# Kernel optimization log

Hardware: AMD Instinct MI355X
Metric: run time of the kernel (lower is better)

The kernel has to match this reference:

```python
import jax, jax.numpy as jnp
import numpy as np

BS, L, ED = 4, 2048, 1024
D = ED // 2          # time_embedding_dim = 512
ANG_HID = D // 4     # AngleEmb hidden = 128
T_MAX = 1010


def _gelu(x):
    return jax.nn.gelu(x, approximate=False)  # torch F.gelu default = exact erf


def _time_embed(t, w1, b1, w2, b2):
    # sinusoidal (diffusion-style, base 10000) + 2-layer MLP; t: [N] float
    half = D // 2
    freqs = jnp.exp(-jnp.log(10000.0) * jnp.arange(half, dtype=jnp.float32) / half)
    a = t[:, None] * freqs[None, :]
    e = jnp.concatenate([jnp.sin(a), jnp.cos(a)], axis=-1)  # [N, D]
    return _gelu(e @ w1 + b1) @ w2 + b2


def _cal_dist(p, aa_seq):
    # p: [bs, L, 3]; ragged per-segment mean pairwise distance.
    # Segments run (cls_idx+1 .. eos_idx-1]; token 0 = cls, token 2 = eos.
    cls = (aa_seq == 0)
    eos = (aa_seq == 2)
    seg = jnp.cumsum(cls.astype(jnp.int32), axis=1)                       # segment id
    valid = (seg > jnp.cumsum(eos.astype(jnp.int32), axis=1)) & ~cls & ~eos
    same = (seg[:, :, None] == seg[:, None, :]) & valid[:, :, None] & valid[:, None, :]
    diff = p[:, :, None, :] - p[:, None, :, :]                            # [bs,L,L,3]
    sq = jnp.sum(diff * diff, axis=-1)
    d = jnp.where(sq > 0, jnp.sqrt(jnp.where(sq > 0, sq, 1.0)), 0.0)      # safe norm
    cnt = jnp.sum(same, axis=-1)                                           # segment size (incl self)
    dist = jnp.where(valid, jnp.sum(d * same, axis=-1) / jnp.maximum(cnt, 1), 0.0)
    return dist[..., None]                                                 # [bs,L,1]


def setup_inputs() -> dict:
    key = jax.random.key(0)
    ks = jax.random.split(key, 26)
    # build ragged aa_seq: repeated [cls=0, residues in [3,25), eos=2], pad token 1
    rng = np.random.default_rng(0)
    aa = np.ones((BS, L), dtype=np.int64)
    pad = np.ones((BS, L), dtype=bool)
    for b in range(BS):
        i = 0
        while i < L - 8:
            seg = int(rng.integers(16, 64))
            seg = min(seg, L - i - 2)
            aa[b, i] = 0
            aa[b, i + 1:i + 1 + seg] = rng.integers(3, 25, size=seg)
            aa[b, i + 1 + seg] = 2
            pad[b, i:i + 2 + seg] = False
            i += seg + 2
    s = 0.05
    inp = {
        "pos": jax.random.normal(ks[0], (BS, L, 3, 3), jnp.float32) * 5.0,
        "angle": jax.random.uniform(ks[1], (BS, L, 6), jnp.float32, -3.14, 3.14),
        "padding_mask": jnp.asarray(pad),
        "mask_aa": jax.random.bernoulli(ks[2], 0.15, (BS, L, 1)),
        "mask_pos": jax.random.bernoulli(ks[3], 0.15, (BS, L, 1)),
        "mask_angle": jax.random.bernoulli(ks[4], 0.15, (BS, L, 1)),
        "angle_mask": jax.random.bernoulli(ks[5], 0.9, (BS, L, 3)),
        "bond_angle_mask": jax.random.bernoulli(ks[6], 0.9, (BS, L, 3)),
        "time_pos": jax.random.randint(ks[7], (BS, L), 0, T_MAX).astype(jnp.float32),
        "time_angle": jnp.zeros((BS, L, 6), jnp.float32),  # overwritten in fwd (dim-2 path)
        "aa_seq": jnp.asarray(aa),
        # parameters ([in, out] layout; torch Linear bias=False unless noted)
        "ang_w1": jax.random.normal(ks[8], (1, ANG_HID), jnp.float32) * 0.5,
        "ang_w2": jax.random.normal(ks[9], (ANG_HID, D), jnp.float32) * s,
        "pos_w1": jax.random.normal(ks[10], (1, 1), jnp.float32) * 0.5,
        "pos_w2": jax.random.normal(ks[11], (1, D), jnp.float32) * s,
        "te_w1": jax.random.normal(ks[12], (D, D), jnp.float32) * s,
        "te_b1": jnp.zeros((D,), jnp.float32),
        "te_w2": jax.random.normal(ks[13], (D, D), jnp.float32) * s,
        "te_b2": jnp.zeros((D,), jnp.float32),
        "angproj_w": jax.random.normal(ks[14], (6 * D, D), jnp.float32) * s,
        "angproj_b": jnp.zeros((D,), jnp.float32),
        "posproj_w": jax.random.normal(ks[15], (D, D), jnp.float32) * s,
        "posproj_b": jnp.zeros((D,), jnp.float32),
        "cls_w": jax.random.normal(ks[16], (1, ED), jnp.float32) * s,
        "eos_w": jax.random.normal(ks[17], (1, ED), jnp.float32) * s,
        "unkang_w": jax.random.normal(ks[18], (1, D), jnp.float32) * s,
        "unkpos_w": jax.random.normal(ks[19], (1, D), jnp.float32) * s,
    }
    return inp


def reference(pos, angle, padding_mask, mask_aa, mask_pos, mask_angle,
              angle_mask, bond_angle_mask, time_pos, time_angle, aa_seq,
              ang_w1, ang_w2, pos_w1, pos_w2,
              te_w1, te_b1, te_w2, te_b2,
              angproj_w, angproj_b, posproj_w, posproj_b,
              cls_w, eos_w, unkang_w, unkpos_w):
    bs, nnode, _ = angle.shape
    amask = jnp.concatenate([angle_mask[:, :, :3], bond_angle_mask], axis=-1)  # [bs,L,6]
    ang = jnp.where(amask, angle, 0.0).reshape(bs, -1, 1)                      # [bs,6L,1]
    cls_mask = (aa_seq == 0)[..., None]
    eos_mask = (aa_seq == 2)[..., None]

    angle_feat = _gelu(ang @ ang_w1) @ ang_w2                                  # [bs,6L,D]
    angle_feat = jnp.where(amask.reshape(bs, -1, 1), angle_feat, unkang_w[0])

    dist = _cal_dist(pos[:, :, 1, :], aa_seq)                                  # [bs,L,1]
    pos_feat = _gelu(dist @ pos_w1) @ pos_w2                                   # [bs,L,D]
    pos_mask = ~(cls_mask | eos_mask)
    pos_feat = jnp.where(pos_mask, pos_feat, unkpos_w[0])

    # time_pos is 2-D -> [bs,L,1]; time_angle := time_pos repeated to [bs,L,6]
    ta = jnp.where(amask, jnp.broadcast_to(time_pos[..., None], (bs, nnode, 6)), 0.0)
    temb_pos = _time_embed(time_pos.reshape(-1), te_w1, te_b1, te_w2, te_b2).reshape(bs, -1, D)
    temb_ang = _time_embed(ta.reshape(-1), te_w1, te_b1, te_w2, te_b2).reshape(bs, -1, D)
    t0_emb = _time_embed(jnp.zeros((1,), jnp.float32), te_w1, te_b1, te_w2, te_b2)[0]  # all-zero t rows are identical

    t_mask = mask_angle & ~cls_mask & ~eos_mask                                # [bs,L,1]
    temb_ang = jnp.where(jnp.tile(t_mask, (1, 6, 1)), temb_ang, t0_emb)        # torch .repeat(1,6,1)
    temb_pos = jnp.where(t_mask, temb_pos, t0_emb)
    angle_feat = angle_feat + temb_ang
    pos_feat = pos_feat + temb_pos

    angle_feat = angle_feat.reshape(bs, nnode, 6 * D) @ angproj_w + angproj_b  # [bs,L,D]
    pos_feat = pos_feat @ posproj_w + posproj_b                                # [bs,L,D]
    node = jnp.concatenate([angle_feat, pos_feat], axis=-1)                    # [bs,L,ED]
    node = jnp.where(cls_mask, cls_w[0], node)
    node = jnp.where(eos_mask, eos_w[0], node)
    node = jnp.where(padding_mask[..., None], 0.0, node)
    return node
```

## Files before the change

kernel.cpp:

```cpp
#include <hip/hip_runtime.h>
#include <hip/hip_bf16.h>
#include <cstdint>
#include <cstddef>

#define BSZ 4
#define SEQL 2048
#define DDIM 512
#define AHID 128
#define NROWS (BSZ*SEQL)
#define NANG (NROWS*6)
#define KCAT 768
#define NTT 1024
#define YCAP 4096

typedef __attribute__((ext_vector_type(8))) short short8;
typedef __attribute__((ext_vector_type(4))) float f32x4;
typedef __hip_bfloat16 bf16;

__device__ __forceinline__ float gelu_f(float x){
  return 0.5f * x * (1.0f + erff(x * 0.7071067811865475f));
}

__device__ __forceinline__ void gload16(const void* g, void* l){
  __builtin_amdgcn_global_load_lds(
      (const __attribute__((address_space(1))) unsigned int*)g,
      (__attribute__((address_space(3))) unsigned int*)l,
      16, 0, 0);
}

__device__ __forceinline__ unsigned int packbf2(float a, float b){
  __hip_bfloat16 ha = __float2bfloat16(a), hb = __float2bfloat16(b);
  return (unsigned int)(*(unsigned short*)&ha) | ((unsigned int)(*(unsigned short*)&hb) << 16);
}

__global__ void pre_kernel(const int* __restrict__ aa, const float* __restrict__ pos,
                           float4* __restrict__ pk,
                           const float* __restrict__ te_w1, const float* __restrict__ te_b1,
                           const float* __restrict__ te_w2, const float* __restrict__ te_b2,
                           const float* __restrict__ angproj_w, const float* __restrict__ posproj_w,
                           const float* __restrict__ unkang, const float* __restrict__ pos_w2,
                           float* __restrict__ t0, float* __restrict__ U,
                           float* __restrict__ Wg, float* __restrict__ qb){
  int blk = blockIdx.x, tid = threadIdx.x;
  if (blk == 0){
    int b = tid >> 6, lane = tid & 63;
    const int CH = SEQL/64;
    int base = b*SEQL + lane*CH;
    int av[CH];
    int lc=0, le=0;
    #pragma unroll
    for (int i=0;i<CH;i++){ int a=aa[base+i]; av[i]=a; lc += (a==0); le += (a==2); }
    int pc=lc, pe=le;
    #pragma unroll
    for (int off=1; off<64; off<<=1){
      int tc = __shfl_up(pc, off);
      int te = __shfl_up(pe, off);
      if (lane >= off){ pc += tc; pe += te; }
    }
    int c = pc - lc, eo = pe - le;
    #pragma unroll
    for (int i=0;i<CH;i++){
      int a = av[i];
      c += (a==0); eo += (a==2);
      bool valid = (c>eo) && (a!=0) && (a!=2);
      float4 q;
      q.x = pos[(size_t)(base+i)*9+3];
      q.y = pos[(size_t)(base+i)*9+4];
      q.z = pos[(size_t)(base+i)*9+5];
      q.w = valid ? (float)c : -1.f;
      pk[base+i] = q;
    }
    return;
  }
  int q = blk - 1;
  if (q < 32){
    __shared__ float zsh[8][32];
    __shared__ float hsh[32];
    int nc = q >> 4, dc = q & 15;
    int d0 = dc * 32;
    int dl = tid & 31, kc = tid >> 5;
    float p = 0.f;
    #pragma unroll 4
    for (int i=0;i<32;i++)
      p += te_w1[(size_t)(256 + kc*32 + i)*512 + d0 + dl];
    zsh[kc][dl] = p;
    __syncthreads();
    if (tid < 32){
      float z = te_b1[d0 + tid];
      #pragma unroll
      for (int k=0;k<8;k++) z += zsh[k][tid];
      hsh[tid] = gelu_f(z);
    }
    __syncthreads();
    int n = nc*256 + tid;
    float s = (dc==0) ? te_b2[n] : 0.f;
    #pragma unroll 4
    for (int i=0;i<32;i++)
      s += hsh[i] * te_w2[(size_t)(d0+i)*512 + n];
    atomicAdd(t0 + n, s);
    return;
  }
  q -= 32;
  if (q < 96){
    int j = q >> 4, rem = q & 15;
    int nc = rem >> 3, dc = rem & 7;
    int n = nc*256 + tid, d0 = dc*64;
    float s = 0.f;
    #pragma unroll 4
    for (int i=0;i<64;i++)
      s += unkang[d0+i] * angproj_w[((size_t)(j*512 + d0+i))*512 + n];
    atomicAdd(U + j*512 + n, s);
    return;
  }
  q -= 96;
  if (q < 16){
    int nc = q >> 3, dc = q & 7;
    int n = nc*256 + tid, d0 = dc*64;
    float s = 0.f;
    #pragma unroll 4
    for (int i=0;i<64;i++)
      s += pos_w2[d0+i] * posproj_w[(size_t)(d0+i)*512 + n];
    atomicAdd(Wg + n, s);
    return;
  }
  q -= 16;
  {
    int j = q >> 4, rem = q & 15;
    int nc = rem >> 3, dc = rem & 7;
    int n = nc*256 + tid, d0 = dc*64;
    const float* W = (j<6) ? (angproj_w + (size_t)(j*512)*512) : posproj_w;
    float s = 0.f;
    #pragma unroll 4
    for (int i=0;i<64;i++)
      s += te_b2[d0+i] * W[(size_t)(d0+i)*512 + n];
    atomicAdd(qb + j*512 + n, s);
  }
}

#define NB_ANGH 3072
#define NB_SIN  256
#define NB_TR   2208
#define NB_PREP 32
#define NB_CONST 112
#define NB_DIST 2048
#define NB_TOTAL (NB_ANGH+NB_SIN+NB_TR+NB_PREP+NB_CONST+NB_DIST)

__device__ void do_transpose(const float* __restrict__ W, bf16* __restrict__ Wt,
                             int K, int q, float (*tsh)[33]){
  int k0 = (q >> 4)*32, n0 = (q & 15)*32;
  int tx = threadIdx.x & 31, ty = threadIdx.x >> 5;
  #pragma unroll
  for (int i=0;i<32;i+=8)
    tsh[ty+i][tx] = W[(size_t)(k0+ty+i)*512 + n0+tx];
  __syncthreads();
  #pragma unroll
  for (int i=0;i<32;i+=8)
    Wt[(size_t)(n0+ty+i)*K + k0+tx] = __float2bfloat16(tsh[tx][ty+i]);
}

__device__ __forceinline__ void wave_append(int j, bool q, int bl,
                                            int* __restrict__ cnts, int* __restrict__ lists,
                                            int* __restrict__ posi){
  unsigned long long m = __ballot(q);
  if (m){
    int lane = threadIdx.x & 63;
    int lead = __ffsll((long long)m) - 1;
    int base = 0;
    if (lane == lead) base = atomicAdd(&cnts[j], __popcll(m));
    base = __shfl(base, lead);
    if (q){
      int pre = __popcll(m & ((1ull<<lane)-1ull));
      int p = base + pre;
      lists[j*NROWS + p] = bl;
      posi[j*NROWS + bl] = p;
    }
  }
}

__global__ void prologue_kernel(const float* __restrict__ angle,
                                const int* __restrict__ angm, const int* __restrict__ bondm,
                                const int* __restrict__ mask_angle, const int* __restrict__ aa,
                                const int* __restrict__ padm,
                                const float* __restrict__ ang_w1,
                                const float* __restrict__ te_w1, const float* __restrict__ te_w2,
                                const float* __restrict__ ang_w2, const float* __restrict__ angproj_w,
                                const float* __restrict__ posproj_w,
                                const float4* __restrict__ pk, const float* __restrict__ t0,
                                bf16* __restrict__ Hang, bf16* __restrict__ et,
                                bf16* __restrict__ tw1t, bf16* __restrict__ apjt,
                                bf16* __restrict__ ppjt, bf16* __restrict__ w2b,
                                bf16* __restrict__ tw2b,
                                unsigned char* __restrict__ amb, unsigned char* __restrict__ scb,
                                int* __restrict__ cnts, int* __restrict__ lists,
                                int* __restrict__ posi,
                                float* __restrict__ dist,
                                float* __restrict__ V, float* __restrict__ Wt0){
  __shared__ float tsh[32][33];
  int blk = blockIdx.x;
  int tid = threadIdx.x;
  if (blk < NB_ANGH){
    int gidx = blk*256 + tid;
    int row = gidx >> 4;
    int kb = (gidx & 15) * 8;
    int bq = row / (SEQL*6);
    int rr = row - bq*(SEQL*6);
    int l = rr / 6, j = rr - l*6;
    int bl = bq*SEQL + l;
    int m = (j<3) ? angm[bl*3+j] : bondm[bl*3+(j-3)];
    float x = m ? angle[bl*6+j] : 0.f;
    float4 w0 = *(const float4*)(ang_w1+kb);
    float4 w1v = *(const float4*)(ang_w1+kb+4);
    uint4 st;
    st.x = packbf2(gelu_f(x*w0.x),  gelu_f(x*w0.y));
    st.y = packbf2(gelu_f(x*w0.z),  gelu_f(x*w0.w));
    st.z = packbf2(gelu_f(x*w1v.x), gelu_f(x*w1v.y));
    st.w = packbf2(gelu_f(x*w1v.z), gelu_f(x*w1v.w));
    *(uint4*)(Hang + (size_t)row*AHID + kb) = st;
    return;
  }
  blk -= NB_ANGH;
  if (blk < NB_SIN){
    int gidx = blk*256 + tid;
    int row = gidx >> 6;
    int db = (gidx & 63) * 8;
    float t = (float)row;
    float v[8];
    #pragma unroll
    for (int i=0;i<8;i++){
      int d = db + i;
      int k = d & 255;
      float f = exp2f(-0.05190512648262f * (float)k);
      float a = t * f;
      v[i] = (d < 256) ? __sinf(a) : __cosf(a);
    }
    uint4 st;
    st.x = packbf2(v[0],v[1]); st.y = packbf2(v[2],v[3]);
    st.z = packbf2(v[4],v[5]); st.w = packbf2(v[6],v[7]);
    *(uint4*)(et + (size_t)row*DDIM + db) = st;
    return;
  }
  blk -= NB_SIN;
  if (blk < NB_TR){
    if (blk < 256)       do_transpose(te_w1, tw1t, 512, blk, tsh);
    else if (blk < 1792) do_transpose(angproj_w, apjt, 3072, blk-256, tsh);
    else if (blk < 2048) do_transpose(posproj_w, ppjt, 512, blk-1792, tsh);
    else if (blk < 2080){
      int gidx = (blk-2048)*256 + tid;
      float4 a0 = *(const float4*)(ang_w2 + (size_t)gidx*8);
      float4 a1 = *(const float4*)(ang_w2 + (size_t)gidx*8 + 4);
      uint4 st;
      st.x = packbf2(a0.x,a0.y); st.y = packbf2(a0.z,a0.w);
      st.z = packbf2(a1.x,a1.y); st.w = packbf2(a1.z,a1.w);
      *(uint4*)(w2b + (size_t)gidx*8) = st;
    } else {
      int gidx = (blk-2080)*256 + tid;
      float4 a0 = *(const float4*)(te_w2 + (size_t)gidx*8);
      float4 a1 = *(const float4*)(te_w2 + (size_t)gidx*8 + 4);
      uint4 st;
      st.x = packbf2(a0.x,a0.y); st.y = packbf2(a0.z,a0.w);
      st.z = packbf2(a1.x,a1.y); st.w = packbf2(a1.z,a1.w);
      *(uint4*)(tw2b + (size_t)gidx*8) = st;
    }
    return;
  }
  blk -= NB_TR;
  if (blk < NB_PREP){
    int bl = blk*256 + tid;
    int b = bl >> 11, l = bl & (SEQL-1);
    int a = aa[bl];
    bool rowOK = (a!=0) && (a!=2) && (padm[bl]==0);
    int ab=0, sb=0;
    #pragma unroll
    for (int j=0;j<6;j++){
      int am = (j<3) ? angm[bl*3+j] : bondm[bl*3+(j-3)];
      int rr = l*6 + j;
      int bl2 = b*SEQL + (rr & (SEQL-1));
      int a2 = aa[bl2];
      bool tm = mask_angle[bl2] && (a2!=0) && (a2!=2);
      bool qs = tm && (am!=0) && rowOK;
      if (am)  ab |= (1<<j);
      if (qs)  sb |= (1<<j);
      wave_append(j, qs, bl, cnts, lists, posi);
    }
    bool q6 = (mask_angle[bl]!=0) && rowOK;
    if (q6) sb |= 64;
    wave_append(6, q6, bl, cnts, lists, posi);
    amb[bl] = (unsigned char)ab;
    scb[bl] = (unsigned char)sb;
    return;
  }
  blk -= NB_PREP;
  if (blk < NB_CONST){
    int j = blk >> 4, rem = blk & 15;
    int nc = rem >> 3, dc = rem & 7;
    int n = nc*256 + tid, d0 = dc*64;
    const float* W = (j<6) ? (angproj_w + (size_t)(j*512)*512) : posproj_w;
    float* dst = (j<6) ? (V + j*512) : Wt0;
    float s = 0.f;
    #pragma unroll 4
    for (int i=0;i<64;i++)
      s += t0[d0+i] * W[(size_t)(d0+i)*512 + n];
    atomicAdd(dst + n, s);
    return;
  }
  blk -= NB_CONST;
  {
    int gw = blk*4 + (tid >> 6);
    int lane = tid & 63;
    float4 c = pk[gw];
    float out = 0.f;
    if (c.w >= 0.f){
      int rowbase = (gw >> 11) << 11;
      int jlo = gw - 64; if (jlo < rowbase) jlo = rowbase;
      int jhi = gw + 64; if (jhi >= rowbase + SEQL) jhi = rowbase + SEQL - 1;
      float s = 0.f, cnt = 0.f;
      for (int j = gw - 64 + lane; j <= jhi; j += 64){
        if (j < jlo) continue;
        float4 q = pk[j];
        if (q.w == c.w){
          float dx = c.x-q.x, dy = c.y-q.y, dz = c.z-q.z;
          float sq = dx*dx+dy*dy+dz*dz;
          s += (sq>0.f) ? sqrtf(sq) : 0.f;
          cnt += 1.f;
        }
      }
      #pragma unroll
      for (int off=32; off>0; off>>=1){
        s   += __shfl_down(s, off);
        cnt += __shfl_down(cnt, off);
      }
      out = s / fmaxf(cnt, 1.f);
    }
    if (lane==0) dist[gw] = out;
  }
}

struct EpiArgs {
  const float* bias;
  const unsigned char* amb;
  const unsigned char* scb;
  const float* U;
  const float* V;
  const float* Y;
  const int* posi;
  const int* aa;
  const int* pad;
  const float* cls;
  const float* eos;
  float* outF;
  bf16* outB;
  int cnt;
  int coloff;
  int ldc;
};

#define STG_BYTES 12288
#define SMEM_BYTES 49152

template<int EPI>
__device__ __forceinline__ void gemm_core(const char* gA, const char* gB,
                                          int K, int bm, int bn, const EpiArgs& ea, char* smem){
  const int tid = threadIdx.x;
  const int w = tid >> 6, lane = tid & 63;
  const bool doB = (w < 4);
  const int wm = (w>>1)*32, wn = (w&1)*32;
  const int lm = lane & 15, kq = lane >> 4;
  const int sw = kq ^ ((lm>>1)&3);
  const int NT = K >> 5;

  f32x4 acc[2][2];
  #pragma unroll
  for (int i=0;i<2;i++)
    #pragma unroll
    for (int j=0;j<2;j++) acc[i][j] = (f32x4){0.f,0.f,0.f,0.f};

  #pragma unroll
  for (int s=0; s<3; ++s){
    char* base = smem + s*STG_BYTES;
    gload16(gA + (size_t)s*64, base + w*1024);
    if (doB) gload16(gB + (size_t)s*64, base + 8192 + w*1024);
  }

  for (int t = 0; t < NT; ++t){
    char* cur = smem + (t&3)*STG_BYTES;
    if (t+3 < NT){
      char* nxt = smem + ((t+3)&3)*STG_BYTES;
      gload16(gA + (size_t)(t+3)*64, nxt + w*1024);
      if (doB) gload16(gB + (size_t)(t+3)*64, nxt + 8192 + w*1024);
    }
    int ia = NT-1-t; if (ia > 3) ia = 3;
    if (doB){
      if      (ia==3) __asm__ volatile("s_waitcnt vmcnt(6)" ::: "memory");
      else if (ia==2) __asm__ volatile("s_waitcnt vmcnt(4)" ::: "memory");
      else if (ia==1) __asm__ volatile("s_waitcnt vmcnt(2)" ::: "memory");
      else            __asm__ volatile("s_waitcnt vmcnt(0)" ::: "memory");
    } else {
      if      (ia==3) __asm__ volatile("s_waitcnt vmcnt(3)" ::: "memory");
      else if (ia==2) __asm__ volatile("s_waitcnt vmcnt(2)" ::: "memory");
      else if (ia==1) __asm__ volatile("s_waitcnt vmcnt(1)" ::: "memory");
      else            __asm__ volatile("s_waitcnt vmcnt(0)" ::: "memory");
    }
    __builtin_amdgcn_s_barrier();
    short8 af[2], bfr[2];
    #pragma unroll
    for (int tt=0;tt<2;tt++) af[tt]  = *(const short8*)(cur + (wm+tt*16+lm)*64 + sw*16);
    #pragma unroll
    for (int tt=0;tt<2;tt++) bfr[tt] = *(const short8*)(cur + 8192 + (wn+tt*16+lm)*64 + sw*16);
    #pragma unroll
    for (int mt=0;mt<2;mt++)
      #pragma unroll
      for (int nt=0;nt<2;nt++)
        acc[mt][nt] = __builtin_amdgcn_mfma_f32_16x16x32_bf16(af[mt], bfr[nt], acc[mt][nt], 0, 0, 0);
    __builtin_amdgcn_s_barrier();
  }

  float* eps = (float*)smem + w*576;
  const int erow = lane >> 2;
  const int ecg  = (lane & 3) * 8;
  #pragma unroll
  for (int mt=0; mt<2; mt++){
    #pragma unroll
    for (int nt=0; nt<2; nt++)
      #pragma unroll
      for (int rr=0; rr<4; rr++)
        eps[(kq*4+rr)*36 + nt*16 + lm] = acc[mt][nt][rr];
    __asm__ volatile("s_waitcnt lgkmcnt(0)" ::: "memory");
    float4 t0v = *(float4*)(eps + erow*36 + ecg);
    float4 t1v = *(float4*)(eps + erow*36 + ecg + 4);
    float v[8] = {t0v.x,t0v.y,t0v.z,t0v.w,t1v.x,t1v.y,t1v.z,t1v.w};
    __asm__ volatile("s_waitcnt lgkmcnt(0)" ::: "memory");
    int row = bm + wm + mt*16 + erow;
    int col = bn + wn + ecg;

    if (EPI==0 || EPI==1){
      float4 b0 = *(const float4*)(ea.bias+col), b1 = *(const float4*)(ea.bias+col+4);
      float bb[8] = {b0.x,b0.y,b0.z,b0.w,b1.x,b1.y,b1.z,b1.w};
      #pragma unroll
      for (int i=0;i<8;i++){
        v[i] += bb[i];
        if (EPI==0) v[i] = gelu_f(v[i]);
      }
      uint4 st;
      st.x = packbf2(v[0],v[1]); st.y = packbf2(v[2],v[3]);
      st.z = packbf2(v[4],v[5]); st.w = packbf2(v[6],v[7]);
      *(uint4*)(ea.outB + (size_t)row*ea.ldc + col) = st;
    } else if (EPI==4){
      uint4 st;
      st.x = packbf2(v[0],v[1]); st.y = packbf2(v[2],v[3]);
      st.z = packbf2(v[4],v[5]); st.w = packbf2(v[6],v[7]);
      *(uint4*)(ea.outB + (size_t)row*ea.ldc + col + ea.coloff) = st;
    } else if (EPI==5){
      float4 b0 = *(const float4*)(ea.bias+col), b1 = *(const float4*)(ea.bias+col+4);
      v[0]+=b0.x; v[1]+=b0.y; v[2]+=b0.z; v[3]+=b0.w;
      v[4]+=b1.x; v[5]+=b1.y; v[6]+=b1.z; v[7]+=b1.w;
      int ab = ea.amb[row], sc = ea.scb[row];
      #pragma unroll
      for (int j=0;j<6;j++){
        float mU = ((ab>>j)&1) ? 0.f : 1.f;
        float mV = ((sc>>j)&1) ? 0.f : 1.f;
        const float* Up = ea.U + j*512 + col;
        const float* Vp = ea.V + j*512 + col;
        float4 u0=*(const float4*)Up, u1=*(const float4*)(Up+4);
        float4 w0=*(const float4*)Vp, w1=*(const float4*)(Vp+4);
        v[0]+=mU*u0.x+mV*w0.x; v[1]+=mU*u0.y+mV*w0.y;
        v[2]+=mU*u0.z+mV*w0.z; v[3]+=mU*u0.w+mV*w0.w;
        v[4]+=mU*u1.x+mV*w1.x; v[5]+=mU*u1.y+mV*w1.y;
        v[6]+=mU*u1.z+mV*w1.z; v[7]+=mU*u1.w+mV*w1.w;
      }
      if (sc & 63){
        #pragma unroll
        for (int j=0;j<6;j++){
          if ((sc>>j)&1){
            const float* yp = ea.Y + ((size_t)j*YCAP + ea.posi[j*NROWS+row])*512 + col;
            float4 y0 = *(const float4*)yp, y1 = *(const float4*)(yp+4);
            v[0]+=y0.x; v[1]+=y0.y; v[2]+=y0.z; v[3]+=y0.w;
            v[4]+=y1.x; v[5]+=y1.y; v[6]+=y1.z; v[7]+=y1.w;
          }
        }
      }
      int a = ea.aa[row];
      if (a==0){
        float4 c0 = *(const float4*)(ea.cls+col), c1 = *(const float4*)(ea.cls+col+4);
        v[0]=c0.x;v[1]=c0.y;v[2]=c0.z;v[3]=c0.w;v[4]=c1.x;v[5]=c1.y;v[6]=c1.z;v[7]=c1.w;
      } else if (a==2){
        float4 c0 = *(const float4*)(ea.eos+col), c1 = *(const float4*)(ea.eos+col+4);
        v[0]=c0.x;v[1]=c0.y;v[2]=c0.z;v[3]=c0.w;v[4]=c1.x;v[5]=c1.y;v[6]=c1.z;v[7]=c1.w;
      }
      if (ea.pad[row]){
        #pragma unroll
        for (int i=0;i<8;i++) v[i]=0.f;
      }
      *(float4*)(ea.outF + (size_t)row*ea.ldc + col)     = make_float4(v[0],v[1],v[2],v[3]);
      *(float4*)(ea.outF + (size_t)row*ea.ldc + col + 4) = make_float4(v[4],v[5],v[6],v[7]);
    } else {
      if (row < ea.cnt){
        float4 b0 = *(const float4*)(ea.bias+col), b1 = *(const float4*)(ea.bias+col+4);
        v[0]+=b0.x; v[1]+=b0.y; v[2]+=b0.z; v[3]+=b0.w;
        v[4]+=b1.x; v[5]+=b1.y; v[6]+=b1.z; v[7]+=b1.w;
        float* dst = ea.outF + (size_t)row*ea.ldc + col;
        *(float4*)dst     = make_float4(v[0],v[1],v[2],v[3]);
        *(float4*)(dst+4) = make_float4(v[4],v[5],v[6],v[7]);
      }
    }
  }
}

__device__ __forceinline__ void mk_addrs(const bf16* A, size_t lda, int bm,
                                         const bf16* Bt, size_t ldb, int bn,
                                         const char*& gA, const char*& gB){
  int tid = threadIdx.x;
  int w = tid >> 6, lane = tid & 63;
  int r = w*16 + (lane>>2);
  int cg = (lane&3) ^ ((r>>1)&3);
  gA = (const char*)(A + (size_t)(bm+r)*lda + cg*8);
  gB = (const char*)(Bt + (size_t)(bn+r)*ldb + cg*8);
}

__launch_bounds__(512, 8)
__global__ void te1_wcat_q_kernel(const bf16* __restrict__ et, const bf16* __restrict__ tw1t,
                                  EpiArgs eaH,
                                  const bf16* __restrict__ apjt, const bf16* __restrict__ ppjt,
                                  const bf16* __restrict__ w2b, const bf16* __restrict__ tw2b,
                                  EpiArgs eaW, bf16* __restrict__ QT){
  __shared__ __align__(16) char smem[SMEM_BYTES];
  int id = blockIdx.x;
  const char *gA, *gB;
  if (id < 64){
    int m = id >> 3, n = id & 7;
    mk_addrs(et, 512, m*128, tw1t, 512, n*64, gA, gB);
    gemm_core<0>(gA, gB, 512, m*128, n*64, eaH, smem);
  } else if (id < 112){
    int q = id - 64;
    int j = q >> 3, m = (q >> 1) & 3, n = q & 1;
    mk_addrs(apjt, 3072, m*128, w2b, 512, n*64, gA, gB);
    gA += (size_t)j*512*2;
    eaW.coloff = j*128;
    gemm_core<4>(gA, gB, 512, m*128, n*64, eaW, smem);
  } else {
    int q = id - 112;
    int j = q >> 5, rem = q & 31;
    int m = rem >> 3, n = rem & 7;
    if (j < 6){
      mk_addrs(apjt, 3072, m*128, tw2b, 512, n*64, gA, gB);
      gA += (size_t)j*512*2;
    } else {
      mk_addrs(ppjt, 512, m*128, tw2b, 512, n*64, gA, gB);
    }
    EpiArgs ea{};
    ea.outB = QT + (size_t)j*DDIM*DDIM; ea.ldc = DDIM; ea.coloff = 0;
    gemm_core<4>(gA, gB, 512, m*128, n*64, ea, smem);
  }
}

__launch_bounds__(512, 8)
__global__ void sparse_kernel(const bf16* __restrict__ H1, const bf16* __restrict__ QT,
                              const float* __restrict__ qb, const float* __restrict__ time_pos,
                              const int* __restrict__ cnts, const int* __restrict__ lists,
                              float* __restrict__ Y){
  __shared__ __align__(16) char smem[SMEM_BYTES];
  int id = blockIdx.x;
  int jj = id >> 8, q = id & 255;
  int mt = q >> 3, nt = q & 7;
  int cnt = cnts[jj];
  if (cnt > YCAP) cnt = YCAP;
  if (mt*128 >= cnt) return;
  const int* idx = lists + jj*NROWS;
  int tid = threadIdx.x;
  int w = tid >> 6, lane = tid & 63;
  int r = w*16 + (lane>>2);
  int cg = (lane&3) ^ ((r>>1)&3);
  int ar = mt*128 + r; if (ar >= cnt) ar = cnt-1;
  int ti = (int)time_pos[idx[ar]];
  const char* gA = (const char*)(H1 + (size_t)ti*DDIM + cg*8);
  const char* gB = (const char*)(QT + (size_t)jj*DDIM*DDIM + (size_t)(nt*64+r)*DDIM + cg*8);
  EpiArgs ea{};
  ea.bias = qb + jj*512;
  ea.cnt = cnt;
  ea.outF = Y + (size_t)jj*YCAP*512;
  ea.ldc = 512;
  gemm_core<7>(gA, gB, 512, mt*128, nt*64, ea, smem);
}

__launch_bounds__(512, 8)
__global__ void proj_kernel(const bf16* __restrict__ Hang, const bf16* __restrict__ Wcat,
                            EpiArgs eaA,
                            const int* __restrict__ aa, const int* __restrict__ padm,
                            const unsigned char* __restrict__ scb, const int* __restrict__ posi,
                            const float* __restrict__ Y,
                            const float* __restrict__ dist,
                            const float* __restrict__ pw1, const float* __restrict__ Wg,
                            const float* __restrict__ Wt0, const float* __restrict__ bp,
                            const float* __restrict__ cls, const float* __restrict__ eos,
                            float* __restrict__ out){
  __shared__ __align__(16) char smem[SMEM_BYTES];
  int id = blockIdx.x;
  if (id < 512){
    int c = id & 7, q = id >> 3;
    int n = q & 7, mh = q >> 3;
    int m = mh*8 + c;
    const char *gA, *gB;
    mk_addrs(Hang, KCAT, m*128, Wcat, KCAT, n*64, gA, gB);
    gemm_core<5>(gA, gB, KCAT, m*128, n*64, eaA, smem);
    return;
  }
  int gidx = (id-512)*512 + threadIdx.x;
  int row = gidx >> 6;
  int db = (gidx & 63) * 8;
  int a = aa[row];
  float v[8];
  if (a==0 || a==2){
    const float* src = ((a==0) ? cls : eos) + DDIM + db;
    float4 c0 = *(const float4*)src, c1 = *(const float4*)(src+4);
    v[0]=c0.x;v[1]=c0.y;v[2]=c0.z;v[3]=c0.w;v[4]=c1.x;v[5]=c1.y;v[6]=c1.z;v[7]=c1.w;
  } else {
    int sc = scb[row];
    float g = gelu_f(dist[row]*pw1[0]);
    float tmul = (sc & 64) ? 0.f : 1.f;
    float4 g0 = *(const float4*)(Wg+db),  g1 = *(const float4*)(Wg+db+4);
    float4 w0 = *(const float4*)(Wt0+db), w1 = *(const float4*)(Wt0+db+4);
    float4 b0 = *(const float4*)(bp+db),  b1 = *(const float4*)(bp+db+4);
    v[0]=g*g0.x+tmul*w0.x+b0.x; v[1]=g*g0.y+tmul*w0.y+b0.y;
    v[2]=g*g0.z+tmul*w0.z+b0.z; v[3]=g*g0.w+tmul*w0.w+b0.w;
    v[4]=g*g1.x+tmul*w1.x+b1.x; v[5]=g*g1.y+tmul*w1.y+b1.y;
    v[6]=g*g1.z+tmul*w1.z+b1.z; v[7]=g*g1.w+tmul*w1.w+b1.w;
    if (sc & 64){
      const float* yp = Y + ((size_t)6*YCAP + posi[6*NROWS+row])*512 + db;
      float4 y0 = *(const float4*)yp, y1 = *(const float4*)(yp+4);
      v[0]+=y0.x; v[1]+=y0.y; v[2]+=y0.z; v[3]+=y0.w;
      v[4]+=y1.x; v[5]+=y1.y; v[6]+=y1.z; v[7]+=y1.w;
    }
  }
  if (padm[row]){
    #pragma unroll
    for (int i=0;i<8;i++) v[i]=0.f;
  }
  float* dst = out + (size_t)row*1024 + DDIM + db;
  *(float4*)dst     = make_float4(v[0],v[1],v[2],v[3]);
  *(float4*)(dst+4) = make_float4(v[4],v[5],v[6],v[7]);
}

extern "C" void kernel_launch(void* const* d_in, const int* in_sizes, int n_in,
                              void* d_out, int out_size, void* d_ws, size_t ws_size,
                              hipStream_t stream){
  const float* pos        = (const float*)d_in[0];
  const float* angle      = (const float*)d_in[1];
  const int*   padm       = (const int*)d_in[2];
  const int*   mask_angle = (const int*)d_in[5];
  const int*   angle_mask = (const int*)d_in[6];
  const int*   bond_mask  = (const int*)d_in[7];
  const float* time_pos   = (const float*)d_in[8];
  const int*   aa         = (const int*)d_in[10];
  const float* ang_w1     = (const float*)d_in[11];
  const float* ang_w2     = (const float*)d_in[12];
  const float* pos_w1     = (const float*)d_in[13];
  const float* pos_w2     = (const float*)d_in[14];
  const float* te_w1      = (const float*)d_in[15];
  const float* te_b1      = (const float*)d_in[16];
  const float* te_w2      = (const float*)d_in[17];
  const float* te_b2      = (const float*)d_in[18];
  const float* angproj_w  = (const float*)d_in[19];
  const float* angproj_b  = (const float*)d_in[20];
  const float* posproj_w  = (const float*)d_in[21];
  const float* posproj_b  = (const float*)d_in[22];
  const float* cls_w      = (const float*)d_in[23];
  const float* eos_w      = (const float*)d_in[24];
  const float* unkang     = (const float*)d_in[25];

  char* ws = (char*)d_ws;
  size_t off = 0;
  auto alloc = [&](size_t bytes)->char*{
    char* p = ws + off;
    off += (bytes + 255) & ~(size_t)255;
    return p;
  };
  int*   cnts   = (int*)  alloc(256);
  float* t0     = (float*)alloc((size_t)DDIM*4);
  float* U      = (float*)alloc((size_t)6*DDIM*4);
  float* V      = (float*)alloc((size_t)6*DDIM*4);
  float* Wt0    = (float*)alloc((size_t)DDIM*4);
  float* Wg     = (float*)alloc((size_t)DDIM*4);
  float* qb     = (float*)alloc((size_t)7*DDIM*4);
  size_t zbytes = (size_t)((char*)qb - (char*)cnts) + 7*DDIM*4;
  float* dist   = (float*)alloc((size_t)NROWS*4);
  float4* pk    = (float4*)alloc((size_t)NROWS*16);
  unsigned char* amb  = (unsigned char*)alloc(NROWS);
  unsigned char* scb  = (unsigned char*)alloc(NROWS);
  int*   lists  = (int*)  alloc((size_t)7*NROWS*4);
  int*   posi   = (int*)  alloc((size_t)7*NROWS*4);
  bf16*  et     = (bf16*) alloc((size_t)NTT*DDIM*2);
  bf16*  H1     = (bf16*) alloc((size_t)NTT*DDIM*2);
  bf16*  Hang   = (bf16*) alloc((size_t)NANG*AHID*2);
  bf16*  tw1t   = (bf16*) alloc((size_t)DDIM*DDIM*2);
  bf16*  apjt   = (bf16*) alloc((size_t)DDIM*6*DDIM*2);
  bf16*  ppjt   = (bf16*) alloc((size_t)DDIM*DDIM*2);
  bf16*  w2b    = (bf16*) alloc((size_t)AHID*DDIM*2);
  bf16*  tw2b   = (bf16*) alloc((size_t)DDIM*DDIM*2);
  bf16*  Wcat   = (bf16*) alloc((size_t)DDIM*KCAT*2);
  bf16*  QT     = (bf16*) alloc((size_t)7*DDIM*DDIM*2);
  float* Y      = (float*)alloc((size_t)7*YCAP*512*4);

  float* out = (float*)d_out;
  dim3 b256(256), b512(512);

  hipMemsetAsync(cnts, 0, zbytes, stream);

  pre_kernel<<<dim3(257), b256, 0, stream>>>(aa, pos, pk,
      te_w1, te_b1, te_w2, te_b2, angproj_w, posproj_w, unkang, pos_w2,
      t0, U, Wg, qb);

  prologue_kernel<<<dim3(NB_TOTAL), b256, 0, stream>>>(
      angle, angle_mask, bond_mask, mask_angle, aa, padm, ang_w1,
      te_w1, te_w2, ang_w2, angproj_w, posproj_w, pk, t0,
      Hang, et, tw1t, apjt, ppjt, w2b, tw2b, amb, scb, cnts, lists, posi,
      dist, V, Wt0);

  EpiArgs eaH{}; eaH.bias = te_b1; eaH.outB = H1; eaH.ldc = DDIM;
  EpiArgs eaW{}; eaW.outB = Wcat; eaW.ldc = KCAT;
  te1_wcat_q_kernel<<<dim3(336), b512, 0, stream>>>(et, tw1t, eaH,
      apjt, ppjt, w2b, tw2b, eaW, QT);

  sparse_kernel<<<dim3(7*256), b512, 0, stream>>>(H1, QT, qb, time_pos,
      cnts, lists, Y);

  EpiArgs eaA{};
  eaA.bias = angproj_b; eaA.amb = amb; eaA.scb = scb; eaA.U = U; eaA.V = V;
  eaA.Y = Y; eaA.posi = posi;
  eaA.aa = aa; eaA.pad = padm; eaA.cls = cls_w; eaA.eos = eos_w;
  eaA.outF = out; eaA.ldc = 1024;
  proj_kernel<<<dim3(1536), b512, 0, stream>>>(Hang, Wcat, eaA,
      aa, padm, scb, posi, Y, dist, pos_w1, Wg, Wt0, posproj_b, cls_w, eos_w, out);
}
```

Baseline: 210.2 us.

## Precompute projected time-embedding table over all timesteps and gather by index

```diff
diff --git a/kernel.cpp b/kernel.cpp
--- a/kernel.cpp
+++ b/kernel.cpp
@@ -11,7 +11,6 @@
 #define NANG (NROWS*6)
 #define KCAT 768
 #define NTT 1024
-#define YCAP 4096
 
 typedef __attribute__((ext_vector_type(8))) short short8;
 typedef __attribute__((ext_vector_type(4))) float f32x4;
@@ -35,12 +34,11 @@
 
 __global__ void pre_kernel(const int* __restrict__ aa, const float* __restrict__ pos,
                            float4* __restrict__ pk,
-                           const float* __restrict__ te_w1, const float* __restrict__ te_b1,
-                           const float* __restrict__ te_w2, const float* __restrict__ te_b2,
+                           const float* __restrict__ te_b2,
                            const float* __restrict__ angproj_w, const float* __restrict__ posproj_w,
                            const float* __restrict__ unkang, const float* __restrict__ pos_w2,
-                           float* __restrict__ t0, float* __restrict__ U,
-                           float* __restrict__ Wg, float* __restrict__ qb){
+                           float* __restrict__ U, float* __restrict__ Wg,
+                           float* __restrict__ qb){
   int blk = blockIdx.x, tid = threadIdx.x;
   if (blk == 0){
     int b = tid >> 6, lane = tid & 63;
@@ -73,34 +71,6 @@
     return;
   }
   int q = blk - 1;
-  if (q < 32){
-    __shared__ float zsh[8][32];
-    __shared__ float hsh[32];
-    int nc = q >> 4, dc = q & 15;
-    int d0 = dc * 32;
-    int dl = tid & 31, kc = tid >> 5;
-    float p = 0.f;
-    #pragma unroll 4
-    for (int i=0;i<32;i++)
-      p += te_w1[(size_t)(256 + kc*32 + i)*512 + d0 + dl];
-    zsh[kc][dl] = p;
-    __syncthreads();
-    if (tid < 32){
-      float z = te_b1[d0 + tid];
-      #pragma unroll
-      for (int k=0;k<8;k++) z += zsh[k][tid];
-      hsh[tid] = gelu_f(z);
-    }
-    __syncthreads();
-    int n = nc*256 + tid;
-    float s = (dc==0) ? te_b2[n] : 0.f;
-    #pragma unroll 4
-    for (int i=0;i<32;i++)
-      s += hsh[i] * te_w2[(size_t)(d0+i)*512 + n];
-    atomicAdd(t0 + n, s);
-    return;
-  }
-  q -= 32;
   if (q < 96){
     int j = q >> 4, rem = q & 15;
     int nc = rem >> 3, dc = rem & 7;
@@ -141,9 +111,8 @@
 #define NB_SIN  256
 #define NB_TR   2208
 #define NB_PREP 32
-#define NB_CONST 112
 #define NB_DIST 2048
-#define NB_TOTAL (NB_ANGH+NB_SIN+NB_TR+NB_PREP+NB_CONST+NB_DIST)
+#define NB_TOTAL (NB_ANGH+NB_SIN+NB_TR+NB_PREP+NB_DIST)
 
 __device__ void do_transpose(const float* __restrict__ W, bf16* __restrict__ Wt,
                              int K, int q, float (*tsh)[33]){
@@ -158,25 +127,6 @@
     Wt[(size_t)(n0+ty+i)*K + k0+tx] = __float2bfloat16(tsh[tx][ty+i]);
 }
 
-__device__ __forceinline__ void wave_append(int j, bool q, int bl,
-                                            int* __restrict__ cnts, int* __restrict__ lists,
-                                            int* __restrict__ posi){
-  unsigned long long m = __ballot(q);
-  if (m){
-    int lane = threadIdx.x & 63;
-    int lead = __ffsll((long long)m) - 1;
-    int base = 0;
-    if (lane == lead) base = atomicAdd(&cnts[j], __popcll(m));
-    base = __shfl(base, lead);
-    if (q){
-      int pre = __popcll(m & ((1ull<<lane)-1ull));
-      int p = base + pre;
-      lists[j*NROWS + p] = bl;
-      posi[j*NROWS + bl] = p;
-    }
-  }
-}
-
 __global__ void prologue_kernel(const float* __restrict__ angle,
                                 const int* __restrict__ angm, const int* __restrict__ bondm,
                                 const int* __restrict__ mask_angle, const int* __restrict__ aa,
@@ -185,16 +135,13 @@
                                 const float* __restrict__ te_w1, const float* __restrict__ te_w2,
                                 const float* __restrict__ ang_w2, const float* __restrict__ angproj_w,
                                 const float* __restrict__ posproj_w,
-                                const float4* __restrict__ pk, const float* __restrict__ t0,
+                                const float4* __restrict__ pk,
                                 bf16* __restrict__ Hang, bf16* __restrict__ et,
                                 bf16* __restrict__ tw1t, bf16* __restrict__ apjt,
                                 bf16* __restrict__ ppjt, bf16* __restrict__ w2b,
                                 bf16* __restrict__ tw2b,
                                 unsigned char* __restrict__ amb, unsigned char* __restrict__ scb,
-                                int* __restrict__ cnts, int* __restrict__ lists,
-                                int* __restrict__ posi,
-                                float* __restrict__ dist,
-                                float* __restrict__ V, float* __restrict__ Wt0){
+                                float* __restrict__ dist){
   __shared__ float tsh[32][33];
   int blk = blockIdx.x;
   int tid = threadIdx.x;
@@ -280,30 +227,13 @@
       bool qs = tm && (am!=0) && rowOK;
       if (am)  ab |= (1<<j);
       if (qs)  sb |= (1<<j);
-      wave_append(j, qs, bl, cnts, lists, posi);
-    }
-    bool q6 = (mask_angle[bl]!=0) && rowOK;
-    if (q6) sb |= 64;
-    wave_append(6, q6, bl, cnts, lists, posi);
+    }
+    if ((mask_angle[bl]!=0) && rowOK) sb |= 64;
     amb[bl] = (unsigned char)ab;
     scb[bl] = (unsigned char)sb;
     return;
   }
   blk -= NB_PREP;
-  if (blk < NB_CONST){
-    int j = blk >> 4, rem = blk & 15;
-    int nc = rem >> 3, dc = rem & 7;
-    int n = nc*256 + tid, d0 = dc*64;
-    const float* W = (j<6) ? (angproj_w + (size_t)(j*512)*512) : posproj_w;
-    float* dst = (j<6) ? (V + j*512) : Wt0;
-    float s = 0.f;
-    #pragma unroll 4
-    for (int i=0;i<64;i++)
-      s += t0[d0+i] * W[(size_t)(d0+i)*512 + n];
-    atomicAdd(dst + n, s);
-    return;
-  }
-  blk -= NB_CONST;
   {
     int gw = blk*4 + (tid >> 6);
     int lane = tid & 63;
@@ -340,9 +270,8 @@
   const unsigned char* amb;
   const unsigned char* scb;
   const float* U;
-  const float* V;
   const float* Y;
-  const int* posi;
+  const float* tp;
   const int* aa;
   const int* pad;
   const float* cls;
@@ -454,29 +383,19 @@
       v[0]+=b0.x; v[1]+=b0.y; v[2]+=b0.z; v[3]+=b0.w;
       v[4]+=b1.x; v[5]+=b1.y; v[6]+=b1.z; v[7]+=b1.w;
       int ab = ea.amb[row], sc = ea.scb[row];
+      int trow = (int)ea.tp[row];
       #pragma unroll
       for (int j=0;j<6;j++){
         float mU = ((ab>>j)&1) ? 0.f : 1.f;
-        float mV = ((sc>>j)&1) ? 0.f : 1.f;
         const float* Up = ea.U + j*512 + col;
-        const float* Vp = ea.V + j*512 + col;
         float4 u0=*(const float4*)Up, u1=*(const float4*)(Up+4);
-        float4 w0=*(const float4*)Vp, w1=*(const float4*)(Vp+4);
-        v[0]+=mU*u0.x+mV*w0.x; v[1]+=mU*u0.y+mV*w0.y;
-        v[2]+=mU*u0.z+mV*w0.z; v[3]+=mU*u0.w+mV*w0.w;
-        v[4]+=mU*u1.x+mV*w1.x; v[5]+=mU*u1.y+mV*w1.y;
-        v[6]+=mU*u1.z+mV*w1.z; v[7]+=mU*u1.w+mV*w1.w;
-      }
-      if (sc & 63){
-        #pragma unroll
-        for (int j=0;j<6;j++){
-          if ((sc>>j)&1){
-            const float* yp = ea.Y + ((size_t)j*YCAP + ea.posi[j*NROWS+row])*512 + col;
-            float4 y0 = *(const float4*)yp, y1 = *(const float4*)(yp+4);
-            v[0]+=y0.x; v[1]+=y0.y; v[2]+=y0.z; v[3]+=y0.w;
-            v[4]+=y1.x; v[5]+=y1.y; v[6]+=y1.z; v[7]+=y1.w;
-          }
-        }
+        int idx = ((sc>>j)&1) ? trow : 0;
+        const float* yp = ea.Y + ((size_t)j*NTT + idx)*512 + col;
+        float4 y0=*(const float4*)yp, y1=*(const float4*)(yp+4);
+        v[0]+=mU*u0.x+y0.x; v[1]+=mU*u0.y+y0.y;
+        v[2]+=mU*u0.z+y0.z; v[3]+=mU*u0.w+y0.w;
+        v[4]+=mU*u1.x+y1.x; v[5]+=mU*u1.y+y1.y;
+        v[6]+=mU*u1.z+y1.z; v[7]+=mU*u1.w+y1.w;
       }
       int a = ea.aa[row];
       if (a==0){
@@ -553,30 +472,18 @@
 }
 
 __launch_bounds__(512, 8)
-__global__ void sparse_kernel(const bf16* __restrict__ H1, const bf16* __restrict__ QT,
-                              const float* __restrict__ qb, const float* __restrict__ time_pos,
-                              const int* __restrict__ cnts, const int* __restrict__ lists,
-                              float* __restrict__ Y){
+__global__ void yt_kernel(const bf16* __restrict__ H1, const bf16* __restrict__ QT,
+                          const float* __restrict__ qb, float* __restrict__ YT){
   __shared__ __align__(16) char smem[SMEM_BYTES];
   int id = blockIdx.x;
-  int jj = id >> 8, q = id & 255;
-  int mt = q >> 3, nt = q & 7;
-  int cnt = cnts[jj];
-  if (cnt > YCAP) cnt = YCAP;
-  if (mt*128 >= cnt) return;
-  const int* idx = lists + jj*NROWS;
-  int tid = threadIdx.x;
-  int w = tid >> 6, lane = tid & 63;
-  int r = w*16 + (lane>>2);
-  int cg = (lane&3) ^ ((r>>1)&3);
-  int ar = mt*128 + r; if (ar >= cnt) ar = cnt-1;
-  int ti = (int)time_pos[idx[ar]];
-  const char* gA = (const char*)(H1 + (size_t)ti*DDIM + cg*8);
-  const char* gB = (const char*)(QT + (size_t)jj*DDIM*DDIM + (size_t)(nt*64+r)*DDIM + cg*8);
+  int jj = id >> 6, rem = id & 63;
+  int mt = rem >> 3, nt = rem & 7;
+  const char *gA, *gB;
+  mk_addrs(H1, 512, mt*128, QT + (size_t)jj*DDIM*DDIM, 512, nt*64, gA, gB);
   EpiArgs ea{};
   ea.bias = qb + jj*512;
-  ea.cnt = cnt;
-  ea.outF = Y + (size_t)jj*YCAP*512;
+  ea.cnt = NTT;
+  ea.outF = YT + (size_t)jj*NTT*512;
   ea.ldc = 512;
   gemm_core<7>(gA, gB, 512, mt*128, nt*64, ea, smem);
 }
@@ -585,11 +492,11 @@
 __global__ void proj_kernel(const bf16* __restrict__ Hang, const bf16* __restrict__ Wcat,
                             EpiArgs eaA,
                             const int* __restrict__ aa, const int* __restrict__ padm,
-                            const unsigned char* __restrict__ scb, const int* __restrict__ posi,
-                            const float* __restrict__ Y,
-                            const float* __restrict__ dist,
+                            const unsigned char* __restrict__ scb,
+                            const float* __restrict__ YT,
+                            const float* __restrict__ dist, const float* __restrict__ time_pos,
                             const float* __restrict__ pw1, const float* __restrict__ Wg,
-                            const float* __restrict__ Wt0, const float* __restrict__ bp,
+                            const float* __restrict__ bp,
                             const float* __restrict__ cls, const float* __restrict__ eos,
                             float* __restrict__ out){
   __shared__ __align__(16) char smem[SMEM_BYTES];
@@ -615,20 +522,15 @@
   } else {
     int sc = scb[row];
     float g = gelu_f(dist[row]*pw1[0]);
-    float tmul = (sc & 64) ? 0.f : 1.f;
+    int idx = (sc & 64) ? (int)time_pos[row] : 0;
+    const float* yp = YT + ((size_t)6*NTT + idx)*512 + db;
     float4 g0 = *(const float4*)(Wg+db),  g1 = *(const float4*)(Wg+db+4);
-    float4 w0 = *(const float4*)(Wt0+db), w1 = *(const float4*)(Wt0+db+4);
+    float4 y0 = *(const float4*)yp,       y1 = *(const float4*)(yp+4);
     float4 b0 = *(const float4*)(bp+db),  b1 = *(const float4*)(bp+db+4);
-    v[0]=g*g0.x+tmul*w0.x+b0.x; v[1]=g*g0.y+tmul*w0.y+b0.y;
-    v[2]=g*g0.z+tmul*w0.z+b0.z; v[3]=g*g0.w+tmul*w0.w+b0.w;
-    v[4]=g*g1.x+tmul*w1.x+b1.x; v[5]=g*g1.y+tmul*w1.y+b1.y;
-    v[6]=g*g1.z+tmul*w1.z+b1.z; v[7]=g*g1.w+tmul*w1.w+b1.w;
-    if (sc & 64){
-      const float* yp = Y + ((size_t)6*YCAP + posi[6*NROWS+row])*512 + db;
-      float4 y0 = *(const float4*)yp, y1 = *(const float4*)(yp+4);
-      v[0]+=y0.x; v[1]+=y0.y; v[2]+=y0.z; v[3]+=y0.w;
-      v[4]+=y1.x; v[5]+=y1.y; v[6]+=y1.z; v[7]+=y1.w;
-    }
+    v[0]=g*g0.x+y0.x+b0.x; v[1]=g*g0.y+y0.y+b0.y;
+    v[2]=g*g0.z+y0.z+b0.z; v[3]=g*g0.w+y0.w+b0.w;
+    v[4]=g*g1.x+y1.x+b1.x; v[5]=g*g1.y+y1.y+b1.y;
+    v[6]=g*g1.z+y1.z+b1.z; v[7]=g*g1.w+y1.w+b1.w;
   }
   if (padm[row]){
     #pragma unroll
@@ -673,20 +575,14 @@
     off += (bytes + 255) & ~(size_t)255;
     return p;
   };
-  int*   cnts   = (int*)  alloc(256);
-  float* t0     = (float*)alloc((size_t)DDIM*4);
   float* U      = (float*)alloc((size_t)6*DDIM*4);
-  float* V      = (float*)alloc((size_t)6*DDIM*4);
-  float* Wt0    = (float*)alloc((size_t)DDIM*4);
   float* Wg     = (float*)alloc((size_t)DDIM*4);
   float* qb     = (float*)alloc((size_t)7*DDIM*4);
-  size_t zbytes = (size_t)((char*)qb - (char*)cnts) + 7*DDIM*4;
+  size_t zbytes = (size_t)((char*)qb - (char*)U) + 7*DDIM*4;
   float* dist   = (float*)alloc((size_t)NROWS*4);
   float4* pk    = (float4*)alloc((size_t)NROWS*16);
   unsigned char* amb  = (unsigned char*)alloc(NROWS);
   unsigned char* scb  = (unsigned char*)alloc(NROWS);
-  int*   lists  = (int*)  alloc((size_t)7*NROWS*4);
-  int*   posi   = (int*)  alloc((size_t)7*NROWS*4);
   bf16*  et     = (bf16*) alloc((size_t)NTT*DDIM*2);
   bf16*  H1     = (bf16*) alloc((size_t)NTT*DDIM*2);
   bf16*  Hang   = (bf16*) alloc((size_t)NANG*AHID*2);
@@ -697,36 +593,33 @@
   bf16*  tw2b   = (bf16*) alloc((size_t)DDIM*DDIM*2);
   bf16*  Wcat   = (bf16*) alloc((size_t)DDIM*KCAT*2);
   bf16*  QT     = (bf16*) alloc((size_t)7*DDIM*DDIM*2);
-  float* Y      = (float*)alloc((size_t)7*YCAP*512*4);
+  float* YT     = (float*)alloc((size_t)7*NTT*512*4);
 
   float* out = (float*)d_out;
   dim3 b256(256), b512(512);
 
-  hipMemsetAsync(cnts, 0, zbytes, stream);
-
-  pre_kernel<<<dim3(257), b256, 0, stream>>>(aa, pos, pk,
-      te_w1, te_b1, te_w2, te_b2, angproj_w, posproj_w, unkang, pos_w2,
-      t0, U, Wg, qb);
+  hipMemsetAsync(U, 0, zbytes, stream);
+
+  pre_kernel<<<dim3(225), b256, 0, stream>>>(aa, pos, pk,
+      te_b2, angproj_w, posproj_w, unkang, pos_w2, U, Wg, qb);
 
   prologue_kernel<<<dim3(NB_TOTAL), b256, 0, stream>>>(
       angle, angle_mask, bond_mask, mask_angle, aa, padm, ang_w1,
-      te_w1, te_w2, ang_w2, angproj_w, posproj_w, pk, t0,
-      Hang, et, tw1t, apjt, ppjt, w2b, tw2b, amb, scb, cnts, lists, posi,
-      dist, V, Wt0);
+      te_w1, te_w2, ang_w2, angproj_w, posproj_w, pk,
+      Hang, et, tw1t, apjt, ppjt, w2b, tw2b, amb, scb, dist);
 
   EpiArgs eaH{}; eaH.bias = te_b1; eaH.outB = H1; eaH.ldc = DDIM;
   EpiArgs eaW{}; eaW.outB = Wcat; eaW.ldc = KCAT;
   te1_wcat_q_kernel<<<dim3(336), b512, 0, stream>>>(et, tw1t, eaH,
       apjt, ppjt, w2b, tw2b, eaW, QT);
 
-  sparse_kernel<<<dim3(7*256), b512, 0, stream>>>(H1, QT, qb, time_pos,
-      cnts, lists, Y);
+  yt_kernel<<<dim3(448), b512, 0, stream>>>(H1, QT, qb, YT);
 
   EpiArgs eaA{};
-  eaA.bias = angproj_b; eaA.amb = amb; eaA.scb = scb; eaA.U = U; eaA.V = V;
-  eaA.Y = Y; eaA.posi = posi;
+  eaA.bias = angproj_b; eaA.amb = amb; eaA.scb = scb; eaA.U = U;
+  eaA.Y = YT; eaA.tp = time_pos;
   eaA.aa = aa; eaA.pad = padm; eaA.cls = cls_w; eaA.eos = eos_w;
   eaA.outF = out; eaA.ldc = 1024;
   proj_kernel<<<dim3(1536), b512, 0, stream>>>(Hang, Wcat, eaA,
-      aa, padm, scb, posi, Y, dist, pos_w1, Wg, Wt0, posproj_b, cls_w, eos_w, out);
-}
+      aa, padm, scb, YT, dist, time_pos, pos_w1, Wg, posproj_b, cls_w, eos_w, out);
+}
```

New measurement: 197.1 us. -6.2%, faster.
